# Optimization experiments

Measured on AMD Instinct MI355X. Metric: run time of the kernel, lower is better.

## Reference

```python
import jax, jax.numpy as jnp
import numpy as np

EPS = 1e-8
RESOLUTION = 32
DILATION = 1


def _stencils(resolution=RESOLUTION, dilation=DILATION):
    # interior grid of resolution^2 samples in [-1, 1]^2 (cell centers)
    lin = (np.arange(resolution) + 0.5) / resolution * 2.0 - 1.0
    gy, gx = np.meshgrid(lin, lin, indexing='ij')
    inner = np.stack([gy.ravel(), gx.ravel()], -1).astype(np.float32)
    # perimeter ring dilated outward by `dilation` cells
    scale = (resolution + 2.0 * dilation) / resolution
    mask = np.zeros((resolution, resolution), bool)
    mask[0, :] = mask[-1, :] = mask[:, 0] = mask[:, -1] = True
    outer = (inner[mask.ravel()] * scale).astype(np.float32)
    # append homogeneous coordinate (matches torch.concat with ones)
    s_in = np.concatenate([inner, np.ones((inner.shape[0], 1), np.float32)], -1)
    s_out = np.concatenate([outer, np.ones((outer.shape[0], 1), np.float32)], -1)
    return jnp.asarray(s_in), jnp.asarray(s_out)


def _bilinear(image, pos):
    # image: (H, W); pos: (..., 2) pixel coords (row, col); clamped bilinear
    H, W = image.shape
    i = pos[..., 0]
    j = pos[..., 1]
    i0 = jnp.clip(jnp.floor(i), 0, H - 2).astype(jnp.int32)
    j0 = jnp.clip(jnp.floor(j), 0, W - 2).astype(jnp.int32)
    di = jnp.clip(i - i0, 0.0, 1.0)
    dj = jnp.clip(j - j0, 0.0, 1.0)
    v00 = image[i0, j0]
    v01 = image[i0, j0 + 1]
    v10 = image[i0 + 1, j0]
    v11 = image[i0 + 1, j0 + 1]
    return (v00 * (1 - di) * (1 - dj) + v01 * (1 - di) * dj
            + v10 * di * (1 - dj) + v11 * di * dj)


def setup_inputs() -> dict:
    key = jax.random.key(0)
    k1, k2 = jax.random.split(key)
    S, P = 4, 4096
    H = W = 2048
    u = jax.random.uniform(k1, (S, P, 5), dtype=jnp.float32)
    xy = u[..., :2] * (H - 1)              # centers inside the image
    ab = 4.0 + u[..., 2:4] * 20.0          # half extents in [4, 24] px
    th = u[..., 4:5] * jnp.float32(np.pi)  # angle in [0, pi)
    points = jnp.concatenate([xy, ab, th], axis=-1)
    points_mask = jnp.ones((S, P), dtype=jnp.float32)
    position_energy_map = jax.random.normal(k2, (1, H, W), dtype=jnp.float32)
    stencil_in, stencil_out = _stencils()
    return {"points": points, "points_mask": points_mask,
            "position_energy_map": position_energy_map,
            "stencil_in": stencil_in, "stencil_out": stencil_out}


def reference(points, points_mask, position_energy_map, stencil_in, stencil_out):
    # affine_from_state: (x, y, a, b, theta) -> 2x3 affine, shape (S, P, 2, 3)
    x, y = points[..., 0], points[..., 1]
    a, b = points[..., 2], points[..., 3]
    t = points[..., 4]
    c, s = jnp.cos(t), jnp.sin(t)
    A = jnp.stack([jnp.stack([a * c, -b * s, x], -1),
                   jnp.stack([a * s, b * c, y], -1)], -2)
    # stencil coordinates in image space: (S, P, n_stencil, 2)
    coords_in = jnp.einsum('spij,nj->spni', A, stencil_in)
    coords_out = jnp.einsum('spij,nj->spni', A, stencil_out)
    img = position_energy_map[0]
    in_values = _bilinear(img, coords_in)    # (S, P, n_in)
    out_values = _bilinear(img, coords_out)  # (S, P, n_out)
    # contrast_measure: t-test-like contrast along stencil dim
    m_in, m_out = in_values.mean(-1), out_values.mean(-1)
    v_in = in_values.var(-1, ddof=1)
    v_out = out_values.var(-1, ddof=1)
    contrast = (m_in - m_out) / jnp.sqrt(v_in + v_out + EPS)
    return contrast * points_mask
```

## Files before the change

kernel.cpp:

```cpp
#include <hip/hip_runtime.h>
#include <math.h>


__global__ __launch_bounds__(256) void contrast_kernel_lean(
    const float* __restrict__ points,
    const float* __restrict__ mask,
    const float* __restrict__ img,
    float* __restrict__ out,
    int n_points)
{
    constexpr float fImax = 2046.f;
    constexpr float fJmax = 2046.f;

    const int wave = (int)((blockIdx.x * (unsigned)blockDim.x + threadIdx.x) >> 6);
    const int lane = (int)(threadIdx.x & 63u);
    if (wave >= n_points) return;

    const float* pt = points + (size_t)wave * 5;
    const float px = pt[0];
    const float py = pt[1];
    const float a  = pt[2];
    const float b  = pt[3];
    const float th = pt[4];

    float sn, cs;
    sincosf(th, &sn, &cs);
    const float A00 = a * cs, A01 = -b * sn;
    const float A10 = a * sn, A11 =  b * cs;

    const int   lr = lane >> 3;
    const int   lc = lane & 7;
    const float syb = fmaf((float)lr, 0.0625f, 0.03125f) - 1.0f;
    const float sxb = fmaf((float)lc, 0.0625f, 0.03125f) - 1.0f;

    float s0 = 0.f, q0 = 0.f, s1 = 0.f, q1 = 0.f;
    #pragma unroll 4
    for (int it = 0; it < 16; ++it) {
        const float dr = (float)(it >> 2) * 0.5f;
        const float dc = (float)(it & 3) * 0.5f;
        const float sy = syb + dr;
        const float sx = sxb + dc;
        const float ci = fmaf(A00, sy, fmaf(A01, sx, px));
        const float cj = fmaf(A10, sy, fmaf(A11, sx, py));
        const float fi = fminf(fmaxf(floorf(ci), 0.f), fImax);
        const float fj = fminf(fmaxf(floorf(cj), 0.f), fJmax);
        const float di = fminf(fmaxf(ci - fi, 0.f), 1.f);
        const float dj = fminf(fmaxf(cj - fj, 0.f), 1.f);
        const unsigned idx = ((unsigned)(int)fi << 11) + (unsigned)(int)fj;
        float2 r0, r1;
        __builtin_memcpy(&r0, &img[idx],         sizeof(float2));
        __builtin_memcpy(&r1, &img[idx + 2048u], sizeof(float2));
        const float top = fmaf(r0.y - r0.x, dj, r0.x);
        const float bot = fmaf(r1.y - r1.x, dj, r1.x);
        const float v   = fmaf(bot - top, di, top);
        if (it & 1) { s1 += v; q1 = fmaf(v, v, q1); }
        else        { s0 += v; q0 = fmaf(v, v, q0); }
    }
    float sum_in = s0 + s1;
    float sq_in  = q0 + q1;

    float sum_out = 0.f, sq_out = 0.f;
    #pragma unroll
    for (int base = 0; base < 124; base += 64) {
        const int n = base + lane;
        if (n < 124) {
            int row, col;
            if (n < 32)      { row = 0;                   col = n; }
            else if (n < 92) { row = 1 + ((n - 32) >> 1); col = (n & 1) * 31; }
            else             { row = 31;                  col = n - 92; }
            const float sy  = (fmaf((float)row, 0.0625f, 0.03125f) - 1.0f) * 1.0625f;
            const float sxo = (fmaf((float)col, 0.0625f, 0.03125f) - 1.0f) * 1.0625f;
            const float ci = fmaf(A00, sy, fmaf(A01, sxo, px));
            const float cj = fmaf(A10, sy, fmaf(A11, sxo, py));
            const float fi = fminf(fmaxf(floorf(ci), 0.f), fImax);
            const float fj = fminf(fmaxf(floorf(cj), 0.f), fJmax);
            const float di = fminf(fmaxf(ci - fi, 0.f), 1.f);
            const float dj = fminf(fmaxf(cj - fj, 0.f), 1.f);
            const unsigned idx = ((unsigned)(int)fi << 11) + (unsigned)(int)fj;
            float2 r0, r1;
            __builtin_memcpy(&r0, &img[idx],         sizeof(float2));
            __builtin_memcpy(&r1, &img[idx + 2048u], sizeof(float2));
            const float top = fmaf(r0.y - r0.x, dj, r0.x);
            const float bot = fmaf(r1.y - r1.x, dj, r1.x);
            const float v   = fmaf(bot - top, di, top);
            sum_out += v;
            sq_out = fmaf(v, v, sq_out);
        }
    }

    #pragma unroll
    for (int off = 32; off > 0; off >>= 1) {
        sum_in  += __shfl_xor(sum_in,  off);
        sq_in   += __shfl_xor(sq_in,   off);
        sum_out += __shfl_xor(sum_out, off);
        sq_out  += __shfl_xor(sq_out,  off);
    }

    if (lane == 0) {
        const float ni = 1024.f, no = 124.f;
        const float m_in  = sum_in  / ni;
        const float m_out = sum_out / no;
        const float v_in  = (sq_in  - ni * m_in  * m_in ) / (ni - 1.f);
        const float v_out = (sq_out - no * m_out * m_out) / (no - 1.f);
        const float contrast = (m_in - m_out) / sqrtf(v_in + v_out + 1e-8f);
        out[wave] = contrast * mask[wave];
    }
}

__global__ __launch_bounds__(256) void contrast_kernel_generic(
    const float* __restrict__ points, const float* __restrict__ mask,
    const float* __restrict__ img, const float* __restrict__ st_in,
    const float* __restrict__ st_out, float* __restrict__ out,
    int n_points, int n_in, int n_out, int Himg, int Wimg)
{
    const int wave = (int)((blockIdx.x * (unsigned)blockDim.x + threadIdx.x) >> 6);
    const int lane = (int)(threadIdx.x & 63u);
    if (wave >= n_points) return;
    const float* pt = points + (size_t)wave * 5;
    const float px = pt[0], py = pt[1], a = pt[2], b = pt[3], th = pt[4];
    float sn, cs; sincosf(th, &sn, &cs);
    const float A00 = a * cs, A01 = -b * sn, A10 = a * sn, A11 = b * cs;
    const float fImax = (float)(Himg - 2), fJmax = (float)(Wimg - 2);
    float sum_in = 0.f, sq_in = 0.f;
    for (int base = 0; base < n_in; base += 64) {
        const int n = base + lane;
        if (n < n_in) {
            const float sy = st_in[n * 3 + 0], sx = st_in[n * 3 + 1];
            const float ci = fmaf(A00, sy, fmaf(A01, sx, px));
            const float cj = fmaf(A10, sy, fmaf(A11, sx, py));
            const float fi = fminf(fmaxf(floorf(ci), 0.f), fImax);
            const float fj = fminf(fmaxf(floorf(cj), 0.f), fJmax);
            const float di = fminf(fmaxf(ci - fi, 0.f), 1.f);
            const float dj = fminf(fmaxf(cj - fj, 0.f), 1.f);
            const float* p0 = img + ((int)fi * Wimg + (int)fj);
            const float v00 = p0[0], v01 = p0[1], v10 = p0[Wimg], v11 = p0[Wimg + 1];
            const float top = fmaf(v01 - v00, dj, v00);
            const float bot = fmaf(v11 - v10, dj, v10);
            const float v = fmaf(bot - top, di, top);
            sum_in += v; sq_in = fmaf(v, v, sq_in);
        }
    }
    float sum_out = 0.f, sq_out = 0.f;
    for (int base = 0; base < n_out; base += 64) {
        const int n = base + lane;
        if (n < n_out) {
            const float sy = st_out[n * 3 + 0], sx = st_out[n * 3 + 1];
            const float ci = fmaf(A00, sy, fmaf(A01, sx, px));
            const float cj = fmaf(A10, sy, fmaf(A11, sx, py));
            const float fi = fminf(fmaxf(floorf(ci), 0.f), fImax);
            const float fj = fminf(fmaxf(floorf(cj), 0.f), fJmax);
            const float di = fminf(fmaxf(ci - fi, 0.f), 1.f);
            const float dj = fminf(fmaxf(cj - fj, 0.f), 1.f);
            const float* p0 = img + ((int)fi * Wimg + (int)fj);
            const float v00 = p0[0], v01 = p0[1], v10 = p0[Wimg], v11 = p0[Wimg + 1];
            const float top = fmaf(v01 - v00, dj, v00);
            const float bot = fmaf(v11 - v10, dj, v10);
            const float v = fmaf(bot - top, di, top);
            sum_out += v; sq_out = fmaf(v, v, sq_out);
        }
    }
    #pragma unroll
    for (int off = 32; off > 0; off >>= 1) {
        sum_in += __shfl_xor(sum_in, off);  sq_in += __shfl_xor(sq_in, off);
        sum_out += __shfl_xor(sum_out, off); sq_out += __shfl_xor(sq_out, off);
    }
    if (lane == 0) {
        const float ni = (float)n_in, no = (float)n_out;
        const float m_in = sum_in / ni, m_out = sum_out / no;
        const float v_in = (sq_in - ni * m_in * m_in) / (ni - 1.f);
        const float v_out = (sq_out - no * m_out * m_out) / (no - 1.f);
        const float contrast = (m_in - m_out) / sqrtf(v_in + v_out + 1e-8f);
        out[wave] = contrast * mask[wave];
    }
}

extern "C" void kernel_launch(void* const* d_in, const int* in_sizes, int n_in_bufs,
                              void* d_out, int out_size, void* d_ws, size_t ws_size,
                              hipStream_t stream) {
    (void)n_in_bufs; (void)d_ws; (void)ws_size; (void)out_size;
    const float* points = (const float*)d_in[0];
    const float* mask   = (const float*)d_in[1];
    const float* img    = (const float*)d_in[2];
    const float* st_in  = (const float*)d_in[3];
    const float* st_out = (const float*)d_in[4];
    float* out = (float*)d_out;

    const int n_points = in_sizes[0] / 5;
    const int n_in     = in_sizes[3] / 3;
    const int n_out    = in_sizes[4] / 3;
    const int hw       = in_sizes[2];

    const int waves_per_block = 4;
    const int blocks = (n_points + waves_per_block - 1) / waves_per_block;

    if (n_in == 1024 && n_out == 124 && hw == 2048 * 2048) {
        contrast_kernel_lean<<<blocks, 256, 0, stream>>>(points, mask, img, out, n_points);
    } else {
        int Wimg = 1;
        while ((long long)Wimg * Wimg < (long long)hw) Wimg <<= 1;
        const int Himg = hw / Wimg;
        contrast_kernel_generic<<<blocks, 256, 0, stream>>>(points, mask, img, st_in, st_out,
                                                            out, n_points, n_in, n_out, Himg, Wimg);
    }
}
```

Before: 113.3 us.

## Stage each point's image footprint in LDS and sample bilinear taps from it

```diff
diff --git a/kernel.cpp b/kernel.cpp
--- a/kernel.cpp
+++ b/kernel.cpp
@@ -2,21 +2,23 @@
 #include <math.h>
 
 
-__global__ __launch_bounds__(256) void contrast_kernel_lean(
+constexpr int TROWS = 58;
+constexpr int TS    = 68;
+
+__global__ __launch_bounds__(64) void contrast_kernel_wtile(
     const float* __restrict__ points,
     const float* __restrict__ mask,
     const float* __restrict__ img,
     float* __restrict__ out,
     int n_points)
 {
-    constexpr float fImax = 2046.f;
-    constexpr float fJmax = 2046.f;
-
-    const int wave = (int)((blockIdx.x * (unsigned)blockDim.x + threadIdx.x) >> 6);
+    __shared__ float tile[TROWS * TS];
+
+    const int pid  = (int)blockIdx.x;
     const int lane = (int)(threadIdx.x & 63u);
-    if (wave >= n_points) return;
-
-    const float* pt = points + (size_t)wave * 5;
+    if (pid >= n_points) return;
+
+    const float* pt = points + (size_t)pid * 5;
     const float px = pt[0];
     const float py = pt[1];
     const float a  = pt[2];
@@ -27,6 +29,30 @@
     sincosf(th, &sn, &cs);
     const float A00 = a * cs, A01 = -b * sn;
     const float A10 = a * sn, A11 =  b * cs;
+
+    const float Ri = (fabsf(A00) + fabsf(A01)) * 1.0625f;
+    const float Rj = (fabsf(A10) + fabsf(A11)) * 1.0625f;
+    const bool use_lds = (Ri <= 28.f) && (Rj <= 28.f);
+
+    int r0 = 0, c0 = 0;
+    if (use_lds) {
+        const int rlo = (int)floorf(px - Ri);
+        const int clo = (int)floorf(py - Rj);
+        r0 = min(max(rlo, 0), 2048 - TROWS);
+        c0 = min(max(clo & ~3, 0), 2048 - 64);
+        const int rhi  = min((int)floorf(px + Ri), 2046);
+        const int rows = min(max(rhi - r0 + 2, 1), TROWS);
+        const int rr = lane >> 4;
+        const int cc = (lane & 15) << 2;
+        for (int base = 0; base < rows; base += 4) {
+            const int rl = base + rr;
+            if (rl < rows) {
+                const float4 v = *reinterpret_cast<const float4*>(
+                    &img[((unsigned)(r0 + rl) << 11) + (unsigned)(c0 + cc)]);
+                *reinterpret_cast<float4*>(&tile[rl * TS + cc]) = v;
+            }
+        }
+    }
 
     const int   lr = lane >> 3;
     const int   lc = lane & 7;
@@ -42,16 +68,24 @@
         const float sx = sxb + dc;
         const float ci = fmaf(A00, sy, fmaf(A01, sx, px));
         const float cj = fmaf(A10, sy, fmaf(A11, sx, py));
-        const float fi = fminf(fmaxf(floorf(ci), 0.f), fImax);
-        const float fj = fminf(fmaxf(floorf(cj), 0.f), fJmax);
+        const float fi = fminf(fmaxf(floorf(ci), 0.f), 2046.f);
+        const float fj = fminf(fmaxf(floorf(cj), 0.f), 2046.f);
         const float di = fminf(fmaxf(ci - fi, 0.f), 1.f);
         const float dj = fminf(fmaxf(cj - fj, 0.f), 1.f);
-        const unsigned idx = ((unsigned)(int)fi << 11) + (unsigned)(int)fj;
-        float2 r0, r1;
-        __builtin_memcpy(&r0, &img[idx],         sizeof(float2));
-        __builtin_memcpy(&r1, &img[idx + 2048u], sizeof(float2));
-        const float top = fmaf(r0.y - r0.x, dj, r0.x);
-        const float bot = fmaf(r1.y - r1.x, dj, r1.x);
+        float v00, v01, v10, v11;
+        if (use_lds) {
+            const int o = ((int)fi - r0) * TS + ((int)fj - c0);
+            v00 = tile[o];      v01 = tile[o + 1];
+            v10 = tile[o + TS]; v11 = tile[o + TS + 1];
+        } else {
+            const unsigned idx = ((unsigned)(int)fi << 11) + (unsigned)(int)fj;
+            float2 t0, t1;
+            __builtin_memcpy(&t0, &img[idx],         sizeof(float2));
+            __builtin_memcpy(&t1, &img[idx + 2048u], sizeof(float2));
+            v00 = t0.x; v01 = t0.y; v10 = t1.x; v11 = t1.y;
+        }
+        const float top = fmaf(v01 - v00, dj, v00);
+        const float bot = fmaf(v11 - v10, dj, v10);
         const float v   = fmaf(bot - top, di, top);
         if (it & 1) { s1 += v; q1 = fmaf(v, v, q1); }
         else        { s0 += v; q0 = fmaf(v, v, q0); }
@@ -72,16 +106,24 @@
             const float sxo = (fmaf((float)col, 0.0625f, 0.03125f) - 1.0f) * 1.0625f;
             const float ci = fmaf(A00, sy, fmaf(A01, sxo, px));
             const float cj = fmaf(A10, sy, fmaf(A11, sxo, py));
-            const float fi = fminf(fmaxf(floorf(ci), 0.f), fImax);
-            const float fj = fminf(fmaxf(floorf(cj), 0.f), fJmax);
+            const float fi = fminf(fmaxf(floorf(ci), 0.f), 2046.f);
+            const float fj = fminf(fmaxf(floorf(cj), 0.f), 2046.f);
             const float di = fminf(fmaxf(ci - fi, 0.f), 1.f);
             const float dj = fminf(fmaxf(cj - fj, 0.f), 1.f);
-            const unsigned idx = ((unsigned)(int)fi << 11) + (unsigned)(int)fj;
-            float2 r0, r1;
-            __builtin_memcpy(&r0, &img[idx],         sizeof(float2));
-            __builtin_memcpy(&r1, &img[idx + 2048u], sizeof(float2));
-            const float top = fmaf(r0.y - r0.x, dj, r0.x);
-            const float bot = fmaf(r1.y - r1.x, dj, r1.x);
+            float v00, v01, v10, v11;
+            if (use_lds) {
+                const int o = ((int)fi - r0) * TS + ((int)fj - c0);
+                v00 = tile[o];      v01 = tile[o + 1];
+                v10 = tile[o + TS]; v11 = tile[o + TS + 1];
+            } else {
+                const unsigned idx = ((unsigned)(int)fi << 11) + (unsigned)(int)fj;
+                float2 t0, t1;
+                __builtin_memcpy(&t0, &img[idx],         sizeof(float2));
+                __builtin_memcpy(&t1, &img[idx + 2048u], sizeof(float2));
+                v00 = t0.x; v01 = t0.y; v10 = t1.x; v11 = t1.y;
+            }
+            const float top = fmaf(v01 - v00, dj, v00);
+            const float bot = fmaf(v11 - v10, dj, v10);
             const float v   = fmaf(bot - top, di, top);
             sum_out += v;
             sq_out = fmaf(v, v, sq_out);
@@ -103,7 +145,7 @@
         const float v_in  = (sq_in  - ni * m_in  * m_in ) / (ni - 1.f);
         const float v_out = (sq_out - no * m_out * m_out) / (no - 1.f);
         const float contrast = (m_in - m_out) / sqrtf(v_in + v_out + 1e-8f);
-        out[wave] = contrast * mask[wave];
+        out[pid] = contrast * mask[pid];
     }
 }
 
@@ -190,15 +232,13 @@
     const int n_out    = in_sizes[4] / 3;
     const int hw       = in_sizes[2];
 
-    const int waves_per_block = 4;
-    const int blocks = (n_points + waves_per_block - 1) / waves_per_block;
-
     if (n_in == 1024 && n_out == 124 && hw == 2048 * 2048) {
-        contrast_kernel_lean<<<blocks, 256, 0, stream>>>(points, mask, img, out, n_points);
+        contrast_kernel_wtile<<<n_points, 64, 0, stream>>>(points, mask, img, out, n_points);
     } else {
         int Wimg = 1;
         while ((long long)Wimg * Wimg < (long long)hw) Wimg <<= 1;
         const int Himg = hw / Wimg;
+        const int blocks = (n_points + 3) / 4;
         contrast_kernel_generic<<<blocks, 256, 0, stream>>>(points, mask, img, st_in, st_out,
                                                             out, n_points, n_in, n_out, Himg, Wimg);
     }
```

New measurement: 130.7 us. 1.15x slower.
